# Kernel tuning notes

Measured on AMD Instinct MI355X. Metric: run time of the kernel, lower is better.

## Reference

```python
import jax, jax.numpy as jnp
import numpy as np

EMBED_DIM = 1024
NUM_HEADS = 16
HEAD_DIM = EMBED_DIM // NUM_HEADS
ROPE_BASE = 10000.0
SQK_INIT_VALUE = 1.0
SQK_INIT_SCALING = 1.0 / (EMBED_DIM ** 0.5)


def setup_inputs() -> dict:
    key = jax.random.key(0)
    ks = jax.random.split(key, 6)
    B, N = 1, 2048
    x = jax.random.normal(ks[0], (B, N, EMBED_DIM), dtype=jnp.float32)
    # torch nn.Linear weights are [out_features, in_features]; y = x @ W.T
    s = EMBED_DIM ** -0.5
    Wq = jax.random.normal(ks[1], (EMBED_DIM, EMBED_DIM), dtype=jnp.float32) * s
    Wk = jax.random.normal(ks[2], (EMBED_DIM, EMBED_DIM), dtype=jnp.float32) * s
    Wv = jax.random.normal(ks[3], (EMBED_DIM, EMBED_DIM), dtype=jnp.float32) * s
    Wo = jax.random.normal(ks[4], (EMBED_DIM, EMBED_DIM), dtype=jnp.float32) * s
    sqk = SQK_INIT_SCALING * jnp.ones((EMBED_DIM,), dtype=jnp.float32) \
        + 0.01 * jax.random.normal(ks[5], (EMBED_DIM,), dtype=jnp.float32)
    return {"x": x, "Wq": Wq, "Wk": Wk, "Wv": Wv, "Wo": Wo, "sqk": sqk}


def _rope(t, offset=0):
    # t: [b, h, n, d]; rotary position embedding (Lrpe type 1), half-split layout
    d = t.shape[-1]
    n = t.shape[-2]
    inv_freq = 1.0 / (ROPE_BASE ** (jnp.arange(0, d, 2, dtype=jnp.float32) / d))  # [d/2]
    pos = jnp.arange(n, dtype=jnp.float32) + offset                               # [n]
    freqs = pos[:, None] * inv_freq[None, :]                                      # [n, d/2]
    cos = jnp.cos(freqs)
    sin = jnp.sin(freqs)
    t1, t2 = jnp.split(t, 2, axis=-1)
    return jnp.concatenate([t1 * cos - t2 * sin, t1 * sin + t2 * cos], axis=-1)


def _justnorm(t):
    return t / jnp.linalg.norm(t, axis=-1, keepdims=True)


def reference(x, Wq, Wk, Wv, Wo, sqk):
    B, N, E = x.shape
    H, D = NUM_HEADS, HEAD_DIM
    q = jnp.einsum('bne,fe->bnf', x, Wq).reshape(B, N, H, D).transpose(0, 2, 1, 3)
    k = jnp.einsum('bne,fe->bnf', x, Wk).reshape(B, N, H, D).transpose(0, 2, 1, 3)
    v = jnp.einsum('bne,fe->bnf', x, Wv).reshape(B, N, H, D).transpose(0, 2, 1, 3)
    q = _rope(q)
    k = _rope(k)
    # sqk * (init_value / init_scaling), reshaped to (h, 1, d)
    sqk_s = (sqk * (SQK_INIT_VALUE / SQK_INIT_SCALING)).reshape(H, 1, D)
    q = sqk_s * _justnorm(q)
    k = sqk_s * _justnorm(k)
    # SDPA with scale = sqrt(head_dim) (as in the source), causal
    scale = D ** 0.5
    scores = jnp.einsum('bhnd,bhmd->bhnm', q, k) * scale
    causal = jnp.tril(jnp.ones((N, N), dtype=bool))
    scores = jnp.where(causal, scores, -jnp.inf)
    attn = jax.nn.softmax(scores, axis=-1)
    out = jnp.einsum('bhnm,bhmd->bhnd', attn, v)           # [b,h,n,d]
    out = out.transpose(0, 2, 1, 3).reshape(B, N, E)       # [b,n,e]
    out = jnp.einsum('bne,fe->bnf', out, Wo)
    return out
```

## Files before the change

kernel.cpp:

```cpp
#include <hip/hip_runtime.h>
#include <hip/hip_bf16.h>

typedef float f32x4 __attribute__((ext_vector_type(4)));
typedef __bf16 bf16x8 __attribute__((ext_vector_type(8)));
typedef __bf16 bf16x4 __attribute__((ext_vector_type(4)));

__device__ __forceinline__ void gload_lds16(const __bf16* g, __bf16* l) {
  __builtin_amdgcn_global_load_lds(
      (const __attribute__((address_space(1))) void*)g,
      (__attribute__((address_space(3))) void*)l, 16, 0, 0);
}

__global__ __launch_bounds__(256) void convert_all(
    const float* __restrict__ x, const float* __restrict__ wq,
    const float* __restrict__ wk, const float* __restrict__ wv,
    const float* __restrict__ wo, __bf16* __restrict__ dst)
{
  int t = blockIdx.x * 256 + threadIdx.x;
  const float* src; size_t soff;
  if (t < 262144) { src = x; soff = (size_t)t * 8; }
  else {
    int r = (t - 262144) >> 17;
    src = (r == 0) ? wq : (r == 1) ? wk : (r == 2) ? wv : wo;
    soff = (size_t)((t - 262144) & 131071) * 8;
  }
  float4 f0 = *(const float4*)(src + soff);
  float4 f1 = *(const float4*)(src + soff + 4);
  bf16x8 o;
  o[0]=(__bf16)f0.x; o[1]=(__bf16)f0.y; o[2]=(__bf16)f0.z; o[3]=(__bf16)f0.w;
  o[4]=(__bf16)f1.x; o[5]=(__bf16)f1.y; o[6]=(__bf16)f1.z; o[7]=(__bf16)f1.w;
  *(bf16x8*)(dst + (size_t)t * 8) = o;
}

template <int BM, int BN, typename OutT, bool ROPE>
__global__ __launch_bounds__(256) void gemm_bt(
    const __bf16* __restrict__ A,
    const __bf16* __restrict__ B0, const __bf16* __restrict__ B1, const __bf16* __restrict__ B2,
    OutT* __restrict__ C0, OutT* __restrict__ C1, OutT* __restrict__ C2,
    int M, int N, int K, const float* __restrict__ sqkp)
{
  const __bf16* B = (blockIdx.z == 0) ? B0 : (blockIdx.z == 1) ? B1 : B2;
  OutT* C = (blockIdx.z == 0) ? C0 : (blockIdx.z == 1) ? C1 : C2;

  constexpr int BK = 64;
  constexpr int MT = BM / 32, NT = BN / 32;
  __shared__ __align__(16) __bf16 As[BM * BK];
  __shared__ __align__(16) __bf16 Bs[BN * BK];

  const int tid = threadIdx.x, w = tid >> 6, l = tid & 63;
  const int wr = w >> 1, wc = w & 1;
  const int g = l >> 4, c16 = l & 15;
  const int bm = blockIdx.y, bn = blockIdx.x;
  const int sr8 = l >> 3, sc = l & 7;

  f32x4 acc[MT][NT] = {};
  const int nk = K >> 6;

  for (int kt = 0; kt < nk; ++kt) {
    __syncthreads();
#pragma unroll
    for (int i = w; i < BM / 8; i += 4) {
      int row = i * 8 + sr8;
      int sch = sc ^ (row & 7);
      gload_lds16(A + (size_t)(bm * BM + row) * K + kt * 64 + sch * 8, As + i * 8 * 64);
    }
#pragma unroll
    for (int i = w; i < BN / 8; i += 4) {
      int row = i * 8 + sr8;
      int sch = sc ^ (row & 7);
      gload_lds16(B + (size_t)(bn * BN + row) * K + kt * 64 + sch * 8, Bs + i * 8 * 64);
    }
    __syncthreads();

    bf16x8 af[MT][2], bf[NT][2];
#pragma unroll
    for (int mt = 0; mt < MT; ++mt) {
      int row = wr * (BM / 2) + mt * 16 + c16;
#pragma unroll
      for (int kk = 0; kk < 2; ++kk)
        af[mt][kk] = *(const bf16x8*)(As + row * 64 + (((kk * 4 + g) ^ (row & 7)) * 8));
    }
#pragma unroll
    for (int nt = 0; nt < NT; ++nt) {
      int row = wc * (BN / 2) + nt * 16 + c16;
#pragma unroll
      for (int kk = 0; kk < 2; ++kk)
        bf[nt][kk] = *(const bf16x8*)(Bs + row * 64 + (((kk * 4 + g) ^ (row & 7)) * 8));
    }
#pragma unroll
    for (int kk = 0; kk < 2; ++kk)
#pragma unroll
      for (int mt = 0; mt < MT; ++mt)
#pragma unroll
        for (int nt = 0; nt < NT; ++nt)
          acc[mt][nt] = __builtin_amdgcn_mfma_f32_16x16x32_bf16(af[mt][kk], bf[nt][kk], acc[mt][nt], 0, 0, 0);
  }

  bool done = false;
  if constexpr (ROPE) {
    static_assert(!ROPE || NT == 4, "ROPE epilogue assumes BN=128 (one head per quadrant)");
    if (blockIdx.z < 2) {
      const bool isQ = (blockIdx.z == 0);
      const int hcol = bn * BN + wc * (BN / 2);
      float sq[4];
#pragma unroll
      for (int nt = 0; nt < 4; ++nt) sq[nt] = sqkp[hcol + nt * 16 + c16] * 32.0f;
      const float QSC = 8.0f * 1.4426950408889634f;
      const float L = 0.415241011860919f;
      const float inv0 = exp2f(-(float)c16 * L);
      const float inv1 = exp2f(-(float)(c16 + 16) * L);
#pragma unroll
      for (int mt = 0; mt < MT; ++mt) {
#pragma unroll
        for (int r = 0; r < 4; ++r) {
          int row = bm * BM + wr * (BM / 2) + mt * 16 + g * 4 + r;
          float s0, c0, s1, c1;
          sincosf((float)row * inv0, &s0, &c0);
          sincosf((float)row * inv1, &s1, &c1);
          float v0 = acc[mt][0][r], v1 = acc[mt][1][r];
          float v2 = acc[mt][2][r], v3 = acc[mt][3][r];
          float n0 = v0 * c0 - v2 * s0;
          float n2 = v0 * s0 + v2 * c0;
          float n1 = v1 * c1 - v3 * s1;
          float n3 = v1 * s1 + v3 * c1;
          float ss = n0 * n0 + n1 * n1 + n2 * n2 + n3 * n3;
#pragma unroll
          for (int m2 = 1; m2 < 16; m2 <<= 1) ss += __shfl_xor(ss, m2, 16);
          float rinv = rsqrtf(ss);
          if (isQ) rinv *= QSC;
          C[(size_t)row * N + hcol +  0 + c16] = (OutT)(n0 * sq[0] * rinv);
          C[(size_t)row * N + hcol + 16 + c16] = (OutT)(n1 * sq[1] * rinv);
          C[(size_t)row * N + hcol + 32 + c16] = (OutT)(n2 * sq[2] * rinv);
          C[(size_t)row * N + hcol + 48 + c16] = (OutT)(n3 * sq[3] * rinv);
        }
      }
      done = true;
    }
  }
  if (!done) {
#pragma unroll
    for (int mt = 0; mt < MT; ++mt)
#pragma unroll
      for (int nt = 0; nt < NT; ++nt)
#pragma unroll
        for (int r = 0; r < 4; ++r) {
          int row = bm * BM + wr * (BM / 2) + mt * 16 + g * 4 + r;
          int col = bn * BN + wc * (BN / 2) + nt * 16 + c16;
          C[(size_t)row * N + col] = (OutT)acc[mt][nt][r];
        }
  }
}

__global__ __launch_bounds__(256) void vtrans(const __bf16* __restrict__ v, __bf16* __restrict__ vt)
{
  __shared__ __align__(16) __bf16 t[64 * 72];
  int h = blockIdx.y;
  int n0 = blockIdx.x * 64;
  int tid = threadIdx.x;
#pragma unroll
  for (int j = 0; j < 2; ++j) {
    int idx = tid + j * 256;
    int r = idx >> 3, c = (idx & 7) * 8;
    bf16x8 val = *(const bf16x8*)(v + (size_t)(n0 + r) * 1024 + h * 64 + c);
    *(bf16x8*)&t[r * 72 + c] = val;
  }
  __syncthreads();
#pragma unroll
  for (int j = 0; j < 2; ++j) {
    int idx = tid + j * 256;
    int d = idx >> 3, nn = (idx & 7) * 8;
    bf16x8 o;
#pragma unroll
    for (int jj = 0; jj < 8; ++jj) o[jj] = t[(nn + jj) * 72 + d];
    *(bf16x8*)(vt + (size_t)(h * 64 + d) * 2048 + n0 + nn) = o;
  }
}

#define STAGE(BUF, KT)                                                         \
  {                                                                            \
    _Pragma("unroll")                                                          \
    for (int p = 0; p < 2; ++p) {                                              \
      int row = srow + p * 32;                                                 \
      int sch = sc ^ (row & 7);                                                \
      gload_lds16(Kg + (size_t)((KT) * 64 + row) * 1024 + h * 64 + sch * 8,    \
                  &Ks[BUF][w * 512 + p * 2048]);                               \
      gload_lds16(Vg + ((size_t)h * 64 + row) * 2048 + (KT) * 64 + sch * 8,    \
                  &Vs[BUF][w * 512 + p * 2048]);                               \
    }                                                                          \
  }

__global__ __launch_bounds__(256, 4) void attn_kernel(
    const __bf16* __restrict__ Qg, const __bf16* __restrict__ Kg,
    const __bf16* __restrict__ Vg, __bf16* __restrict__ Og,
    float* __restrict__ oS, float* __restrict__ lS)
{
  __shared__ __align__(16) __bf16 Ks[2][4096];
  __shared__ __align__(16) __bf16 Vs[2][4096];
  __shared__ __align__(16) __bf16 Ps[4][16 * 72];

  const int b = blockIdx.x;
  int h, qt, kts, kte, sidx;
  if (b < 512) {
    int p = b >> 5;
    qt = 16 + p;
    sidx = (b >> 4) & 1;
    h = b & 15;
    int mid = (qt + 1) >> 1;
    kts = sidx ? mid : 0;
    kte = sidx ? qt : (mid - 1);
  } else {
    qt = 15 - ((b - 512) >> 4);
    h = b & 15;
    kts = 0; kte = qt; sidx = -1;
  }
  const int q0 = qt * 64;

  const int tid = threadIdx.x, w = tid >> 6, l = tid & 63;
  const int g = l >> 4, c16 = l & 15;
  const int srow = tid >> 3;
  const int sc   = tid & 7;

  __bf16* Ps_w = &Ps[w][0];

  const __bf16* qbase = Qg + (size_t)(q0 + w * 16 + c16) * 1024 + h * 64 + g * 8;
  const bf16x8 qf0 = *(const bf16x8*)(qbase);
  const bf16x8 qf1 = *(const bf16x8*)(qbase + 32);

  f32x4 o[4] = {};
  float lsum[4] = {0.f, 0.f, 0.f, 0.f};

  STAGE(0, kts)

  for (int kt = kts; kt <= kte; ++kt) {
    const int cur = (kt - kts) & 1;
    __syncthreads();
    if (kt < kte) STAGE(cur ^ 1, kt + 1)

    const __bf16* Kb = Ks[cur];
    const __bf16* Vb = Vs[cur];

    f32x4 s[4] = {};
#pragma unroll
    for (int nt = 0; nt < 4; ++nt) {
      int r = nt * 16 + c16;
      bf16x8 k0 = *(const bf16x8*)((char*)Kb + r * 128 + ((g ^ (r & 7)) * 16));
      bf16x8 k1 = *(const bf16x8*)((char*)Kb + r * 128 + (((4 + g) ^ (r & 7)) * 16));
      s[nt] = __builtin_amdgcn_mfma_f32_16x16x32_bf16(qf0, k0, s[nt], 0, 0, 0);
      s[nt] = __builtin_amdgcn_mfma_f32_16x16x32_bf16(qf1, k1, s[nt], 0, 0, 0);
    }

    const bool diag = (kt == qt);
#pragma unroll
    for (int r = 0; r < 4; ++r) {
#pragma unroll
      for (int nt = 0; nt < 4; ++nt) {
        float sv = s[nt][r];
        if (diag && (nt * 16 + c16) > (w * 16 + g * 4 + r)) sv = -1e30f;
        float e = exp2f(sv);
        Ps_w[(g * 4 + r) * 72 + nt * 16 + c16] = (__bf16)e;
        lsum[r] += e;
      }
    }

#pragma unroll
    for (int ks = 0; ks < 2; ++ks) {
      bf16x8 pa = *(const bf16x8*)((char*)Ps_w + c16 * 144 + ks * 64 + g * 16);
#pragma unroll
      for (int nt = 0; nt < 4; ++nt) {
        int r = nt * 16 + c16;
        bf16x8 vb = *(const bf16x8*)((char*)Vb + r * 128 + (((ks * 4 + g) ^ (r & 7)) * 16));
        o[nt] = __builtin_amdgcn_mfma_f32_16x16x32_bf16(pa, vb, o[nt], 0, 0, 0);
      }
    }
  }

#pragma unroll
  for (int m2 = 1; m2 < 16; m2 <<= 1) {
#pragma unroll
    for (int r = 0; r < 4; ++r) lsum[r] += __shfl_xor(lsum[r], m2, 16);
  }

  if (sidx < 0) {
#pragma unroll
    for (int r = 0; r < 4; ++r) {
      float rinv = 1.0f / lsum[r];
      int qi = q0 + w * 16 + g * 4 + r;
#pragma unroll
      for (int nt = 0; nt < 4; ++nt)
        Og[(size_t)qi * 1024 + h * 64 + nt * 16 + c16] = (__bf16)(o[nt][r] * rinv);
    }
  } else {
    float* oBase = oS + (size_t)sidx * 1024 * 1024;
#pragma unroll
    for (int r = 0; r < 4; ++r) {
      int row = q0 + w * 16 + g * 4 + r - 1024;
#pragma unroll
      for (int nt = 0; nt < 4; ++nt)
        oBase[(size_t)row * 1024 + h * 64 + nt * 16 + c16] = o[nt][r];
      if (c16 == 0)
        lS[(size_t)sidx * 1024 * 16 + (size_t)row * 16 + h] = lsum[r];
    }
  }
}

__global__ __launch_bounds__(256) void merge_halves(
    const float* __restrict__ oS, const float* __restrict__ lS,
    __bf16* __restrict__ Og)
{
  int row = blockIdx.x;
  int col = threadIdx.x * 4;
  int h = col >> 6;
  float lsum = lS[(size_t)row * 16 + h] + lS[(size_t)(1024 + row) * 16 + h];
  float rinv = 1.0f / lsum;
  f32x4 a = *(const f32x4*)(oS + (size_t)row * 1024 + col);
  f32x4 bb = *(const f32x4*)(oS + (size_t)(1024 * 1024) + (size_t)row * 1024 + col);
  f32x4 sum = a + bb;
  bf16x4 ob;
  ob[0] = (__bf16)(sum[0] * rinv); ob[1] = (__bf16)(sum[1] * rinv);
  ob[2] = (__bf16)(sum[2] * rinv); ob[3] = (__bf16)(sum[3] * rinv);
  *(bf16x4*)(Og + (size_t)(1024 + row) * 1024 + col) = ob;
}

extern "C" void kernel_launch(void* const* d_in, const int* in_sizes, int n_in,
                              void* d_out, int out_size, void* d_ws, size_t ws_size,
                              hipStream_t stream) {
  const float* x   = (const float*)d_in[0];
  const float* Wq  = (const float*)d_in[1];
  const float* Wk  = (const float*)d_in[2];
  const float* Wv  = (const float*)d_in[3];
  const float* Wo  = (const float*)d_in[4];
  const float* sqk = (const float*)d_in[5];
  float* out = (float*)d_out;

  __bf16* xb  = (__bf16*)d_ws;
  __bf16* wqb = xb  + (size_t)2048 * 1024;
  __bf16* wkb = wqb + (size_t)1024 * 1024;
  __bf16* wvb = wkb + (size_t)1024 * 1024;
  __bf16* wob = wvb + (size_t)1024 * 1024;
  __bf16* qn  = wob + (size_t)1024 * 1024;
  __bf16* kn  = qn  + (size_t)2048 * 1024;
  __bf16* v   = kn  + (size_t)2048 * 1024;
  __bf16* vtb = v   + (size_t)2048 * 1024;
  __bf16* og  = vtb + (size_t)2048 * 1024;
  float*  oS  = (float*)(og + (size_t)2048 * 1024);
  float*  lS  = oS + (size_t)2 * 1024 * 1024;

  convert_all<<<3072, 256, 0, stream>>>(x, Wq, Wk, Wv, Wo, xb);
  gemm_bt<64, 128, __bf16, true><<<dim3(8, 32, 3), 256, 0, stream>>>(
      xb, wqb, wkb, wvb, qn, kn, v, 2048, 1024, 1024, sqk);
  vtrans<<<dim3(32, 16), 256, 0, stream>>>(v, vtb);
  attn_kernel<<<768, 256, 0, stream>>>(qn, kn, vtb, og, oS, lS);
  merge_halves<<<1024, 256, 0, stream>>>(oS, lS, og);
  gemm_bt<64, 64, float, false><<<dim3(16, 32, 1), 256, 0, stream>>>(
      og, wob, wob, wob, out, out, out, 2048, 1024, 1024, nullptr);
}
```

Before: 77.38 us.

## Deepen GEMM K tile and transpose attention score layout for vectorized P stores

The GEMM kernel gains a BK template parameter, and both projection GEMMs now use a 128-wide K tile instead of 64. This halves the number of K iterations and barriers, at the cost of twice the LDS per block and possibly lower occupancy. In attention, the score MFMA swaps its operands so each lane owns one query row. Probabilities can then be written to LDS as packed bf16x4, and the row sum is one scalar per lane, reduced with two shuffles instead of a 16-lane shuffle tree over four values. The final normalization reads row sums back through LDS.

After: 77.22 us. Within noise of the previous version (-0.2%).

```diff
diff --git a/kernel.cpp b/kernel.cpp
--- a/kernel.cpp
+++ b/kernel.cpp
@@ -32,7 +32,7 @@
   *(bf16x8*)(dst + (size_t)t * 8) = o;
 }
 
-template <int BM, int BN, typename OutT, bool ROPE>
+template <int BM, int BN, int BK, typename OutT, bool ROPE>
 __global__ __launch_bounds__(256) void gemm_bt(
     const __bf16* __restrict__ A,
     const __bf16* __restrict__ B0, const __bf16* __restrict__ B1, const __bf16* __restrict__ B2,
@@ -42,8 +42,9 @@
   const __bf16* B = (blockIdx.z == 0) ? B0 : (blockIdx.z == 1) ? B1 : B2;
   OutT* C = (blockIdx.z == 0) ? C0 : (blockIdx.z == 1) ? C1 : C2;
 
-  constexpr int BK = 64;
-  constexpr int MT = BM / 32, NT = BN / 32;
+  constexpr int MT = BM / 32, NT = BN / 32, KK = BK / 32;
+  constexpr int CPR = BK / 8;
+  constexpr int RPI = 64 / CPR;
   __shared__ __align__(16) __bf16 As[BM * BK];
   __shared__ __align__(16) __bf16 Bs[BN * BK];
 
@@ -51,54 +52,51 @@
   const int wr = w >> 1, wc = w & 1;
   const int g = l >> 4, c16 = l & 15;
   const int bm = blockIdx.y, bn = blockIdx.x;
-  const int sr8 = l >> 3, sc = l & 7;
+  const int lr = l / CPR, lc = l % CPR;
 
   f32x4 acc[MT][NT] = {};
-  const int nk = K >> 6;
+  const int nk = K / BK;
 
   for (int kt = 0; kt < nk; ++kt) {
     __syncthreads();
 #pragma unroll
-    for (int i = w; i < BM / 8; i += 4) {
-      int row = i * 8 + sr8;
-      int sch = sc ^ (row & 7);
-      gload_lds16(A + (size_t)(bm * BM + row) * K + kt * 64 + sch * 8, As + i * 8 * 64);
-    }
-#pragma unroll
-    for (int i = w; i < BN / 8; i += 4) {
-      int row = i * 8 + sr8;
-      int sch = sc ^ (row & 7);
-      gload_lds16(B + (size_t)(bn * BN + row) * K + kt * 64 + sch * 8, Bs + i * 8 * 64);
+    for (int i = w; i < BM / RPI; i += 4) {
+      int row = i * RPI + lr;
+      int sch = lc ^ (row & 7);
+      gload_lds16(A + (size_t)(bm * BM + row) * K + kt * BK + sch * 8, As + i * RPI * BK);
+    }
+#pragma unroll
+    for (int i = w; i < BN / RPI; i += 4) {
+      int row = i * RPI + lr;
+      int sch = lc ^ (row & 7);
+      gload_lds16(B + (size_t)(bn * BN + row) * K + kt * BK + sch * 8, Bs + i * RPI * BK);
     }
     __syncthreads();
 
-    bf16x8 af[MT][2], bf[NT][2];
-#pragma unroll
-    for (int mt = 0; mt < MT; ++mt) {
-      int row = wr * (BM / 2) + mt * 16 + c16;
-#pragma unroll
-      for (int kk = 0; kk < 2; ++kk)
-        af[mt][kk] = *(const bf16x8*)(As + row * 64 + (((kk * 4 + g) ^ (row & 7)) * 8));
-    }
-#pragma unroll
-    for (int nt = 0; nt < NT; ++nt) {
-      int row = wc * (BN / 2) + nt * 16 + c16;
-#pragma unroll
-      for (int kk = 0; kk < 2; ++kk)
-        bf[nt][kk] = *(const bf16x8*)(Bs + row * 64 + (((kk * 4 + g) ^ (row & 7)) * 8));
-    }
-#pragma unroll
-    for (int kk = 0; kk < 2; ++kk)
+#pragma unroll
+    for (int kk = 0; kk < KK; ++kk) {
+      bf16x8 af[MT], bf[NT];
+#pragma unroll
+      for (int mt = 0; mt < MT; ++mt) {
+        int row = wr * (BM / 2) + mt * 16 + c16;
+        af[mt] = *(const bf16x8*)(As + row * BK + (((kk * 4 + g) ^ (row & 7)) * 8));
+      }
+#pragma unroll
+      for (int nt = 0; nt < NT; ++nt) {
+        int row = wc * (BN / 2) + nt * 16 + c16;
+        bf[nt] = *(const bf16x8*)(Bs + row * BK + (((kk * 4 + g) ^ (row & 7)) * 8));
+      }
 #pragma unroll
       for (int mt = 0; mt < MT; ++mt)
 #pragma unroll
         for (int nt = 0; nt < NT; ++nt)
-          acc[mt][nt] = __builtin_amdgcn_mfma_f32_16x16x32_bf16(af[mt][kk], bf[nt][kk], acc[mt][nt], 0, 0, 0);
+          acc[mt][nt] = __builtin_amdgcn_mfma_f32_16x16x32_bf16(af[mt], bf[nt], acc[mt][nt], 0, 0, 0);
+    }
   }
 
   bool done = false;
   if constexpr (ROPE) {
-    static_assert(!ROPE || NT == 4, "ROPE epilogue assumes BN=128 (one head per quadrant)");
+    static_assert(!ROPE || NT == 4, "ROPE epilogue assumes BN=128");
     if (blockIdx.z < 2) {
       const bool isQ = (blockIdx.z == 0);
       const int hcol = bn * BN + wc * (BN / 2);
@@ -221,13 +219,14 @@
   const int sc   = tid & 7;
 
   __bf16* Ps_w = &Ps[w][0];
-
-  const __bf16* qbase = Qg + (size_t)(q0 + w * 16 + c16) * 1024 + h * 64 + g * 8;
+  const int qig = q0 + w * 16 + c16;
+
+  const __bf16* qbase = Qg + (size_t)qig * 1024 + h * 64 + g * 8;
   const bf16x8 qf0 = *(const bf16x8*)(qbase);
   const bf16x8 qf1 = *(const bf16x8*)(qbase + 32);
 
   f32x4 o[4] = {};
-  float lsum[4] = {0.f, 0.f, 0.f, 0.f};
+  float lsum = 0.f;
 
   STAGE(0, kts)
 
@@ -241,25 +240,28 @@
 
     f32x4 s[4] = {};
 #pragma unroll
-    for (int nt = 0; nt < 4; ++nt) {
-      int r = nt * 16 + c16;
+    for (int kjb = 0; kjb < 4; ++kjb) {
+      int r = kjb * 16 + c16;
       bf16x8 k0 = *(const bf16x8*)((char*)Kb + r * 128 + ((g ^ (r & 7)) * 16));
       bf16x8 k1 = *(const bf16x8*)((char*)Kb + r * 128 + (((4 + g) ^ (r & 7)) * 16));
-      s[nt] = __builtin_amdgcn_mfma_f32_16x16x32_bf16(qf0, k0, s[nt], 0, 0, 0);
-      s[nt] = __builtin_amdgcn_mfma_f32_16x16x32_bf16(qf1, k1, s[nt], 0, 0, 0);
+      s[kjb] = __builtin_amdgcn_mfma_f32_16x16x32_bf16(k0, qf0, s[kjb], 0, 0, 0);
+      s[kjb] = __builtin_amdgcn_mfma_f32_16x16x32_bf16(k1, qf1, s[kjb], 0, 0, 0);
     }
 
     const bool diag = (kt == qt);
 #pragma unroll
-    for (int r = 0; r < 4; ++r) {
-#pragma unroll
-      for (int nt = 0; nt < 4; ++nt) {
-        float sv = s[nt][r];
-        if (diag && (nt * 16 + c16) > (w * 16 + g * 4 + r)) sv = -1e30f;
+    for (int kjb = 0; kjb < 4; ++kjb) {
+      bf16x4 pk;
+#pragma unroll
+      for (int r = 0; r < 4; ++r) {
+        float sv = s[kjb][r];
+        int kvg = kt * 64 + kjb * 16 + g * 4 + r;
+        if (diag && kvg > qig) sv = -1e30f;
         float e = exp2f(sv);
-        Ps_w[(g * 4 + r) * 72 + nt * 16 + c16] = (__bf16)e;
-        lsum[r] += e;
-      }
+        pk[r] = (__bf16)e;
+        lsum += e;
+      }
+      *(bf16x4*)((char*)Ps_w + c16 * 144 + kjb * 32 + g * 8) = pk;
     }
 
 #pragma unroll
@@ -274,16 +276,16 @@
     }
   }
 
-#pragma unroll
-  for (int m2 = 1; m2 < 16; m2 <<= 1) {
-#pragma unroll
-    for (int r = 0; r < 4; ++r) lsum[r] += __shfl_xor(lsum[r], m2, 16);
-  }
+  lsum += __shfl_xor(lsum, 16);
+  lsum += __shfl_xor(lsum, 32);
 
   if (sidx < 0) {
+    float* lsh = (float*)Ps_w;
+    if (g == 0) lsh[c16] = lsum;
+    __builtin_amdgcn_s_waitcnt(0);
 #pragma unroll
     for (int r = 0; r < 4; ++r) {
-      float rinv = 1.0f / lsum[r];
+      float rinv = 1.0f / lsh[g * 4 + r];
       int qi = q0 + w * 16 + g * 4 + r;
 #pragma unroll
       for (int nt = 0; nt < 4; ++nt)
@@ -297,9 +299,9 @@
 #pragma unroll
       for (int nt = 0; nt < 4; ++nt)
         oBase[(size_t)row * 1024 + h * 64 + nt * 16 + c16] = o[nt][r];
-      if (c16 == 0)
-        lS[(size_t)sidx * 1024 * 16 + (size_t)row * 16 + h] = lsum[r];
-    }
+    }
+    if (g == 0)
+      lS[(size_t)sidx * 1024 * 16 + (size_t)(qig - 1024) * 16 + h] = lsum;
   }
 }
 
@@ -346,11 +348,11 @@
   float*  lS  = oS + (size_t)2 * 1024 * 1024;
 
   convert_all<<<3072, 256, 0, stream>>>(x, Wq, Wk, Wv, Wo, xb);
-  gemm_bt<64, 128, __bf16, true><<<dim3(8, 32, 3), 256, 0, stream>>>(
+  gemm_bt<64, 128, 128, __bf16, true><<<dim3(8, 32, 3), 256, 0, stream>>>(
       xb, wqb, wkb, wvb, qn, kn, v, 2048, 1024, 1024, sqk);
   vtrans<<<dim3(32, 16), 256, 0, stream>>>(v, vtb);
   attn_kernel<<<768, 256, 0, stream>>>(qn, kn, vtb, og, oS, lS);
   merge_halves<<<1024, 256, 0, stream>>>(oS, lS, og);
-  gemm_bt<64, 64, float, false><<<dim3(16, 32, 1), 256, 0, stream>>>(
+  gemm_bt<64, 64, 128, float, false><<<dim3(16, 32, 1), 256, 0, stream>>>(
       og, wob, wob, wob, out, out, out, 2048, 1024, 1024, nullptr);
 }
```
